# Kernel tuning notes

Measured on AMD Instinct MI355X. Metric: run time of the kernel, lower is better.

Reference implementation:

```python
import jax, jax.numpy as jnp
import numpy as np

WS = 7          # window_size
HEADS = 6
HEAD_DIM = 32
DISP = WS // 2  # displacement = 3
NEG = -1e9      # stands in for -inf in shift masks (safe for grads/low precision)


def _rel_indices():
    # get_relative_distances(window_size) + window_size - 1
    pos = np.array([[i, j] for i in range(WS) for j in range(WS)])  # (49, 2)
    return pos[None, :, :] - pos[:, None, :] + WS - 1               # (49, 49, 2)


def _shift_mask(nw_h, nw_w):
    # per-window additive mask replicating upper_lower_mask / left_right_mask placement
    n = WS * WS
    ul = np.zeros((n, n), np.float32)
    ul[-DISP * WS:, :-DISP * WS] = NEG
    ul[:-DISP * WS, -DISP * WS:] = NEG
    m4 = np.zeros((WS, WS, WS, WS), np.float32)
    m4[:, -DISP:, :, :-DISP] = NEG
    m4[:, :-DISP, :, -DISP:] = NEG
    lr = m4.reshape(n, n)
    full = np.zeros((nw_h, nw_w, n, n), np.float32)
    full[-1, :] += ul              # dots[:, :, -nw_w:] += upper_lower_mask
    full[:, -1] += lr              # dots[:, :, nw_w-1::nw_w] += left_right_mask
    return full.reshape(nw_h * nw_w, n, n)


def setup_inputs() -> dict:
    key = jax.random.key(0)
    k1, k2, k3, k4 = jax.random.split(key, 4)
    dim, inner = 192, HEADS * HEAD_DIM
    return {
        "x": jax.random.normal(k1, (16, 56, 56, dim), jnp.float32),
        "w_qkv": jax.random.normal(k2, (dim, inner * 3), jnp.float32) * 0.02,
        "pos_embedding": jax.random.normal(k3, (2 * WS - 1, 2 * WS - 1), jnp.float32),
        "w_out": jax.random.normal(k4, (inner, dim), jnp.float32) * 0.02,
        "b_out": jnp.zeros((dim,), jnp.float32),
    }


def reference(x, w_qkv, pos_embedding, w_out, b_out):
    b, H, W, dim = x.shape
    nw_h, nw_w = H // WS, W // WS
    x = jnp.roll(x, (-DISP, -DISP), axis=(1, 2))          # shifted window
    qkv = x @ w_qkv                                       # [b,H,W,3*inner]
    q, k, v = jnp.split(qkv, 3, axis=-1)

    def to_windows(t):  # [b,H,W,inner] -> [b,h,nw,ws*ws,d]
        t = t.reshape(b, nw_h, WS, nw_w, WS, HEADS, HEAD_DIM)
        return t.transpose(0, 5, 1, 3, 2, 4, 6).reshape(b, HEADS, nw_h * nw_w, WS * WS, HEAD_DIM)

    q, k, v = to_windows(q), to_windows(k), to_windows(v)
    scale = HEAD_DIM ** -0.5
    dots = jnp.einsum('bhwid,bhwjd->bhwij', q, k) * scale  # [b,h,nw,49,49]

    rel = _rel_indices()
    bias = pos_embedding[rel[..., 0], rel[..., 1]]         # [49,49]
    dots = dots + bias
    dots = dots + jnp.asarray(_shift_mask(nw_h, nw_w))     # broadcast over b,h

    attn = jax.nn.softmax(dots, axis=-1)
    out = jnp.einsum('bhwij,bhwjd->bhwid', attn, v)        # [b,h,nw,49,d]
    out = out.reshape(b, HEADS, nw_h, nw_w, WS, WS, HEAD_DIM)
    out = out.transpose(0, 2, 4, 3, 5, 1, 6).reshape(b, H, W, HEADS * HEAD_DIM)
    out = out @ w_out + b_out
    return jnp.roll(out, (DISP, DISP), axis=(1, 2))
```

## Files before the change

kernel.cpp:

```cpp
#include <hip/hip_runtime.h>
#include <hip/hip_bf16.h>

typedef __bf16 bf16_t;
typedef __bf16 bf16x8 __attribute__((ext_vector_type(8)));
typedef float f32x4 __attribute__((ext_vector_type(4)));
typedef unsigned int u32;

#define NB 16
#define HW 56
#define DIM 192
#define N3 576
#define WS7 7
#define HEADS 6
#define HD 32
#define NTOK 49
#define MFMA(a, b, c) __builtin_amdgcn_mfma_f32_16x16x32_bf16(a, b, c, 0, 0, 0)

__device__ __forceinline__ void gld_lds16(const bf16_t* g, bf16_t* l) {
    __builtin_amdgcn_global_load_lds((const __attribute__((address_space(1))) u32*)g,
                                     (__attribute__((address_space(3))) u32*)l, 16, 0, 0);
}

__global__ __launch_bounds__(256) void prep_x_kernel(const float* __restrict__ x,
                                                     bf16_t* __restrict__ xb) {
    int idx = blockIdx.x * 256 + threadIdx.x;
    const int total = NB * HW * HW * (DIM / 8);
    if (idx >= total) return;
    int c8 = idx % (DIM / 8);
    int p  = idx / (DIM / 8);
    int xx = p % HW;
    int yy = (p / HW) % HW;
    int bb = p / (HW * HW);
    int ys = yy + 3; if (ys >= HW) ys -= HW;
    int xs = xx + 3; if (xs >= HW) xs -= HW;
    const float* src = x + ((size_t)(bb * HW + ys) * HW + xs) * DIM + c8 * 8;
    float4 a0 = *reinterpret_cast<const float4*>(src);
    float4 a1 = *reinterpret_cast<const float4*>(src + 4);
    bf16x8 o;
    o[0] = (bf16_t)a0.x; o[1] = (bf16_t)a0.y; o[2] = (bf16_t)a0.z; o[3] = (bf16_t)a0.w;
    o[4] = (bf16_t)a1.x; o[5] = (bf16_t)a1.y; o[6] = (bf16_t)a1.z; o[7] = (bf16_t)a1.w;
    *reinterpret_cast<bf16x8*>(xb + (size_t)idx * 8) = o;
}

__global__ __launch_bounds__(256) void prep_w_kernel(const float* __restrict__ wqkv,
                                                     const float* __restrict__ wout,
                                                     bf16_t* __restrict__ wqkvt,
                                                     bf16_t* __restrict__ woutt) {
    int idx = blockIdx.x * 256 + threadIdx.x;
    if (idx < N3 * DIM) {
        int k = idx % DIM, n = idx / DIM;
        wqkvt[idx] = (bf16_t)wqkv[(size_t)k * N3 + n];
    } else {
        int j = idx - N3 * DIM;
        if (j < DIM * DIM) {
            int k = j % DIM, n = j / DIM;
            woutt[j] = (bf16_t)wout[(size_t)k * DIM + n];
        }
    }
}

__global__ __launch_bounds__(256) void prep_tbl_kernel(const float* __restrict__ pe,
                                                       float* __restrict__ tbl) {
    int idx = blockIdx.x * 256 + threadIdx.x;
    if (idx >= 4 * 64 * 64) return;
    int v = idx >> 12, rem = idx & 4095, ti = rem >> 6, tj = rem & 63;
    float val = -1e9f;
    if (ti < NTOK && tj < NTOK) {
        int yi = ti / 7, xi = ti % 7, yj = tj / 7, xj = tj % 7;
        val = pe[(yj - yi + 6) * 13 + (xj - xi + 6)];
        bool mr = (v & 2) && ((yi >= 4) != (yj >= 4));
        bool mc = (v & 1) && ((xi >= 4) != (xj >= 4));
        if (mr || mc) val = -1e9f;
    }
    tbl[idx] = val;
}

__global__ __launch_bounds__(256) void fused_attn_kernel2(const bf16_t* __restrict__ xb,
                                                          const bf16_t* __restrict__ wt,
                                                          const float* __restrict__ tbl,
                                                          bf16_t* __restrict__ att) {
    const int h = blockIdx.x, win = blockIdx.y, bb = blockIdx.z;
    const int wh = win >> 3, ww = win & 7;
    const int mt = threadIdx.x >> 6;
    const int lane = threadIdx.x & 63;
    const int lo = lane & 15, hi = lane >> 4;

    __shared__ alignas(16) bf16_t WL[96 * DIM];
    __shared__ alignas(16) bf16_t Qs[64 * 40];
    __shared__ alignas(16) bf16_t Ks[64 * 40];
    bf16_t* VTs = WL;
    bf16_t* P   = WL + 32 * 72;

#pragma unroll
    for (int i = 0; i < 9; i++) {
        int cbase = i * 256 + mt * 64;
        int cid = cbase + lane;
        int seg = cid / 768;
        int c0 = cid - seg * 768;
        int g0 = c0 ^ ((c0 / 24) & 7);
        gld_lds16(wt + (size_t)(seg * DIM + h * HD) * DIM + g0 * 8,
                  WL + (size_t)cbase * 8);
    }

    bf16x8 a[6];
    {
        int t = mt * 16 + lo;
        if (t >= NTOK) t = 0;
        int y = wh * WS7 + t / 7, xcol = ww * WS7 + t % 7;
        const bf16_t* ar = xb + ((size_t)(bb * HW + y) * HW + xcol) * DIM + hi * 8;
#pragma unroll
        for (int ks = 0; ks < 6; ks++)
            a[ks] = *reinterpret_cast<const bf16x8*>(ar + ks * 32);
    }

    __syncthreads();

    f32x4 acc6[3][2];
#pragma unroll
    for (int s = 0; s < 3; s++)
#pragma unroll
        for (int nt = 0; nt < 2; nt++) acc6[s][nt] = (f32x4){0.f, 0.f, 0.f, 0.f};

#pragma unroll
    for (int s = 0; s < 3; s++)
#pragma unroll
        for (int nt = 0; nt < 2; nt++) {
            int lr = s * 32 + nt * 16 + lo;
            const char* rowp = (const char*)WL + lr * 384;
            int rx = (lr & 7) << 4;
#pragma unroll
            for (int ks = 0; ks < 6; ks++) {
                bf16x8 bf = *reinterpret_cast<const bf16x8*>(rowp + ((ks * 64 + hi * 16) ^ rx));
                acc6[s][nt] = MFMA(a[ks], bf, acc6[s][nt]);
            }
        }

    __syncthreads();

    const float qs = 0.17677669529663687f;
#pragma unroll
    for (int nt = 0; nt < 2; nt++)
#pragma unroll
        for (int r = 0; r < 4; r++) {
            int tok = mt * 16 + hi * 4 + r;
            Qs[tok * 40 + nt * 16 + lo] = (bf16_t)(acc6[0][nt][r] * qs);
            Ks[tok * 40 + nt * 16 + lo] = (bf16_t)acc6[1][nt][r];
            VTs[(nt * 16 + lo) * 72 + tok] = (bf16_t)acc6[2][nt][r];
        }
    __syncthreads();

    const f32x4 zero4 = {0.f, 0.f, 0.f, 0.f};
    bf16x8 qa = *reinterpret_cast<const bf16x8*>(&Qs[(mt * 16 + lo) * 40 + hi * 8]);
    f32x4 s4[4];
#pragma unroll
    for (int ct = 0; ct < 4; ct++) {
        bf16x8 kb = *reinterpret_cast<const bf16x8*>(&Ks[(ct * 16 + lo) * 40 + hi * 8]);
        s4[ct] = MFMA(qa, kb, zero4);
    }

    const int variant = ((wh == 7) ? 2 : 0) | ((ww == 7) ? 1 : 0);
    const float* tbase = tbl + ((size_t)variant << 12);
    float rinv[4];
#pragma unroll
    for (int r = 0; r < 4; r++) {
        int ti = mt * 16 + hi * 4 + r;
        const float* trow = tbase + ti * 64 + lo;
        float vals[4];
        float mx = -3e38f;
#pragma unroll
        for (int ct = 0; ct < 4; ct++) {
            float v = s4[ct][r] + trow[ct * 16];
            vals[ct] = v;
            mx = fmaxf(mx, v);
        }
#pragma unroll
        for (int off = 1; off < 16; off <<= 1) mx = fmaxf(mx, __shfl_xor(mx, off));
        float sum = 0.f;
#pragma unroll
        for (int ct = 0; ct < 4; ct++) {
            float p = __expf(vals[ct] - mx);
            sum += p;
            P[ti * 72 + ct * 16 + lo] = (bf16_t)p;
        }
#pragma unroll
        for (int off = 1; off < 16; off <<= 1) sum += __shfl_xor(sum, off);
        rinv[r] = 1.f / sum;
    }

    f32x4 o[2] = {zero4, zero4};
#pragma unroll
    for (int ks = 0; ks < 2; ks++) {
        bf16x8 pa = *reinterpret_cast<const bf16x8*>(&P[(mt * 16 + lo) * 72 + ks * 32 + hi * 8]);
#pragma unroll
        for (int c2 = 0; c2 < 2; c2++) {
            bf16x8 vb = *reinterpret_cast<const bf16x8*>(&VTs[(c2 * 16 + lo) * 72 + ks * 32 + hi * 8]);
            o[c2] = MFMA(pa, vb, o[c2]);
        }
    }

#pragma unroll
    for (int r = 0; r < 4; r++) {
        int ti = mt * 16 + hi * 4 + r;
        if (ti < NTOK) {
            int y = wh * WS7 + ti / 7, xcol = ww * WS7 + ti % 7;
            size_t aoff = ((size_t)(bb * HW + y) * HW + xcol) * DIM + h * HD;
#pragma unroll
            for (int c2 = 0; c2 < 2; c2++)
                att[aoff + c2 * 16 + lo] = (bf16_t)(o[c2][r] * rinv[r]);
        }
    }
}

__global__ __launch_bounds__(256) void out_gemm2(const bf16_t* __restrict__ att,
                                                 const bf16_t* __restrict__ wt,
                                                 const float* __restrict__ bias,
                                                 float* __restrict__ out) {
    __shared__ alignas(16) bf16_t bsh[64 * DIM];
    const int mblk = blockIdx.x, nblk = blockIdx.y;
    const int wave = threadIdx.x >> 6, lane = threadIdx.x & 63;
    const int lo = lane & 15, hi = lane >> 4;

    const bf16_t* bt = wt + (size_t)nblk * 64 * DIM;
#pragma unroll
    for (int i = 0; i < 6; i++) {
        int s = wave * 384 + i * 64 + lane;
        int g = s ^ ((s / 24) & 7);
        gld_lds16(bt + g * 8, bsh + (wave * 384 + i * 64) * 8);
    }

    bf16x8 a[2][6];
    const bf16_t* ab = att + ((size_t)mblk * 128 + wave * 32 + lo) * DIM + hi * 8;
#pragma unroll
    for (int mt = 0; mt < 2; mt++)
#pragma unroll
        for (int ks = 0; ks < 6; ks++)
            a[mt][ks] = *reinterpret_cast<const bf16x8*>(ab + mt * 16 * DIM + ks * 32);

    f32x4 acc[2][4];
#pragma unroll
    for (int mt = 0; mt < 2; mt++)
#pragma unroll
        for (int ct = 0; ct < 4; ct++) acc[mt][ct] = (f32x4){0.f, 0.f, 0.f, 0.f};

    __syncthreads();

#pragma unroll
    for (int ks = 0; ks < 6; ks++)
#pragma unroll
        for (int ct = 0; ct < 4; ct++) {
            int r = ct * 16 + lo;
            int off = (ks * 64 + hi * 16) ^ ((r & 7) << 4);
            bf16x8 b = *reinterpret_cast<const bf16x8*>((const char*)bsh + r * 384 + off);
            acc[0][ct] = MFMA(a[0][ks], b, acc[0][ct]);
            acc[1][ct] = MFMA(a[1][ks], b, acc[1][ct]);
        }

    const int rb = mblk * 128 + wave * 32;
#pragma unroll
    for (int mt = 0; mt < 2; mt++)
#pragma unroll
        for (int r = 0; r < 4; r++) {
            int m = rb + mt * 16 + hi * 4 + r;
            int bb = m / (HW * HW);
            int rem = m - bb * HW * HW;
            int ya = rem / HW, xa = rem - ya * HW;
            int yo = ya + 3; if (yo >= HW) yo -= HW;
            int xo = xa + 3; if (xo >= HW) xo -= HW;
            size_t ob = ((size_t)(bb * HW + yo) * HW + xo) * DIM + nblk * 64;
#pragma unroll
            for (int ct = 0; ct < 4; ct++)
                out[ob + ct * 16 + lo] = acc[mt][ct][r] + bias[nblk * 64 + ct * 16 + lo];
        }
}

extern "C" void kernel_launch(void* const* d_in, const int* in_sizes, int n_in,
                              void* d_out, int out_size, void* d_ws, size_t ws_size,
                              hipStream_t stream) {
    const float* x    = (const float*)d_in[0];
    const float* wqkv = (const float*)d_in[1];
    const float* pe   = (const float*)d_in[2];
    const float* wout = (const float*)d_in[3];
    const float* bout = (const float*)d_in[4];
    float* out = (float*)d_out;

    char* ws = (char*)d_ws;
    const size_t XB_BYTES  = (size_t)NB * HW * HW * DIM * 2;
    const size_t ATT_BYTES = XB_BYTES;
    const size_t WQ_BYTES  = (size_t)N3 * DIM * 2;
    const size_t WO_BYTES  = (size_t)DIM * DIM * 2;
    bf16_t* xb    = (bf16_t*)ws;
    bf16_t* att   = (bf16_t*)(ws + XB_BYTES);
    bf16_t* wqkvt = (bf16_t*)(ws + XB_BYTES + ATT_BYTES);
    bf16_t* woutt = (bf16_t*)(ws + XB_BYTES + ATT_BYTES + WQ_BYTES);
    float*  tbl   = (float*)(ws + XB_BYTES + ATT_BYTES + WQ_BYTES + WO_BYTES);

    prep_x_kernel<<<(NB * HW * HW * (DIM / 8) + 255) / 256, 256, 0, stream>>>(x, xb);
    prep_w_kernel<<<(N3 * DIM + DIM * DIM + 255) / 256, 256, 0, stream>>>(wqkv, wout, wqkvt, woutt);
    prep_tbl_kernel<<<64, 256, 0, stream>>>(pe, tbl);
    fused_attn_kernel2<<<dim3(HEADS, 64, NB), 256, 0, stream>>>(xb, wqkvt, tbl, att);
    out_gemm2<<<dim3(392, 3), 256, 0, stream>>>(att, woutt, bout, out);
}
```

Baseline: 154.4 us.

## Process four windows per attention block and double output GEMM row tile

The fused attention kernel now loops over four windows per block. It loads the per-head K/V weights into LDS once and keeps the Q weights in registers, so weight staging is amortized across windows, and it prefetches the bias/mask table into registers. VTs and P get dedicated LDS buffers instead of aliasing the weight buffer. The output GEMM doubles its M tile to 256 rows per block, reusing each LDS B-fragment across four MFMA tiles. Grids shrink four-fold and two-fold, which reduces parallelism and raises register pressure.

```diff
diff --git a/kernel.cpp b/kernel.cpp
--- a/kernel.cpp
+++ b/kernel.cpp
@@ -75,143 +75,169 @@
     tbl[idx] = val;
 }
 
-__global__ __launch_bounds__(256) void fused_attn_kernel2(const bf16_t* __restrict__ xb,
+__global__ __launch_bounds__(256) void fused_attn_kernel3(const bf16_t* __restrict__ xb,
                                                           const bf16_t* __restrict__ wt,
                                                           const float* __restrict__ tbl,
                                                           bf16_t* __restrict__ att) {
-    const int h = blockIdx.x, win = blockIdx.y, bb = blockIdx.z;
-    const int wh = win >> 3, ww = win & 7;
+    const int h = blockIdx.x, wq = blockIdx.y, bb = blockIdx.z;
     const int mt = threadIdx.x >> 6;
     const int lane = threadIdx.x & 63;
     const int lo = lane & 15, hi = lane >> 4;
 
-    __shared__ alignas(16) bf16_t WL[96 * DIM];
+    __shared__ alignas(16) bf16_t WL[64 * DIM];
     __shared__ alignas(16) bf16_t Qs[64 * 40];
     __shared__ alignas(16) bf16_t Ks[64 * 40];
-    bf16_t* VTs = WL;
-    bf16_t* P   = WL + 32 * 72;
-
-#pragma unroll
-    for (int i = 0; i < 9; i++) {
+    __shared__ alignas(16) bf16_t VTs[32 * 72];
+    __shared__ alignas(16) bf16_t P[64 * 72];
+
+#pragma unroll
+    for (int i = 0; i < 6; i++) {
         int cbase = i * 256 + mt * 64;
         int cid = cbase + lane;
         int seg = cid / 768;
         int c0 = cid - seg * 768;
         int g0 = c0 ^ ((c0 / 24) & 7);
-        gld_lds16(wt + (size_t)(seg * DIM + h * HD) * DIM + g0 * 8,
+        gld_lds16(wt + (size_t)((seg + 1) * DIM + h * HD) * DIM + g0 * 8,
                   WL + (size_t)cbase * 8);
     }
 
-    bf16x8 a[6];
-    {
-        int t = mt * 16 + lo;
-        if (t >= NTOK) t = 0;
-        int y = wh * WS7 + t / 7, xcol = ww * WS7 + t % 7;
-        const bf16_t* ar = xb + ((size_t)(bb * HW + y) * HW + xcol) * DIM + hi * 8;
+    bf16x8 qw[2][6];
+#pragma unroll
+    for (int nt = 0; nt < 2; nt++) {
+        const bf16_t* bp = wt + (size_t)(h * HD + nt * 16 + lo) * DIM + hi * 8;
 #pragma unroll
         for (int ks = 0; ks < 6; ks++)
-            a[ks] = *reinterpret_cast<const bf16x8*>(ar + ks * 32);
+            qw[nt][ks] = *reinterpret_cast<const bf16x8*>(bp + ks * 32);
     }
 
     __syncthreads();
 
-    f32x4 acc6[3][2];
-#pragma unroll
-    for (int s = 0; s < 3; s++)
-#pragma unroll
-        for (int nt = 0; nt < 2; nt++) acc6[s][nt] = (f32x4){0.f, 0.f, 0.f, 0.f};
-
-#pragma unroll
-    for (int s = 0; s < 3; s++)
-#pragma unroll
-        for (int nt = 0; nt < 2; nt++) {
-            int lr = s * 32 + nt * 16 + lo;
-            const char* rowp = (const char*)WL + lr * 384;
-            int rx = (lr & 7) << 4;
-#pragma unroll
-            for (int ks = 0; ks < 6; ks++) {
-                bf16x8 bf = *reinterpret_cast<const bf16x8*>(rowp + ((ks * 64 + hi * 16) ^ rx));
-                acc6[s][nt] = MFMA(a[ks], bf, acc6[s][nt]);
-            }
-        }
-
-    __syncthreads();
-
     const float qs = 0.17677669529663687f;
-#pragma unroll
-    for (int nt = 0; nt < 2; nt++)
+    const f32x4 zero4 = {0.f, 0.f, 0.f, 0.f};
+
+    for (int w = 0; w < 4; w++) {
+        const int win = wq * 4 + w;
+        const int wh = win >> 3, ww = win & 7;
+
+        bf16x8 a[6];
+        {
+            int t = mt * 16 + lo;
+            if (t >= NTOK) t = 0;
+            int y = wh * WS7 + t / 7, xcol = ww * WS7 + t % 7;
+            const bf16_t* ar = xb + ((size_t)(bb * HW + y) * HW + xcol) * DIM + hi * 8;
+#pragma unroll
+            for (int ks = 0; ks < 6; ks++)
+                a[ks] = *reinterpret_cast<const bf16x8*>(ar + ks * 32);
+        }
+
+        const int variant = ((wh == 7) ? 2 : 0) | ((ww == 7) ? 1 : 0);
+        const float* tbase = tbl + ((size_t)variant << 12);
+        float tv[4][4];
+#pragma unroll
+        for (int r = 0; r < 4; r++)
+#pragma unroll
+            for (int ct = 0; ct < 4; ct++)
+                tv[r][ct] = tbase[(mt * 16 + hi * 4 + r) * 64 + ct * 16 + lo];
+
+        f32x4 acc6[3][2];
+#pragma unroll
+        for (int s = 0; s < 3; s++)
+#pragma unroll
+            for (int nt = 0; nt < 2; nt++) acc6[s][nt] = zero4;
+
+#pragma unroll
+        for (int nt = 0; nt < 2; nt++)
+#pragma unroll
+            for (int ks = 0; ks < 6; ks++)
+                acc6[0][nt] = MFMA(a[ks], qw[nt][ks], acc6[0][nt]);
+
+#pragma unroll
+        for (int s = 1; s < 3; s++)
+#pragma unroll
+            for (int nt = 0; nt < 2; nt++) {
+                int lr = (s - 1) * 32 + nt * 16 + lo;
+                const char* rowp = (const char*)WL + lr * 384;
+                int rx = (lr & 7) << 4;
+#pragma unroll
+                for (int ks = 0; ks < 6; ks++) {
+                    bf16x8 bf = *reinterpret_cast<const bf16x8*>(rowp + ((ks * 64 + hi * 16) ^ rx));
+                    acc6[s][nt] = MFMA(a[ks], bf, acc6[s][nt]);
+                }
+            }
+
+        __syncthreads();
+
+#pragma unroll
+        for (int nt = 0; nt < 2; nt++)
+#pragma unroll
+            for (int r = 0; r < 4; r++) {
+                int tok = mt * 16 + hi * 4 + r;
+                Qs[tok * 40 + nt * 16 + lo] = (bf16_t)(acc6[0][nt][r] * qs);
+                Ks[tok * 40 + nt * 16 + lo] = (bf16_t)acc6[1][nt][r];
+                VTs[(nt * 16 + lo) * 72 + tok] = (bf16_t)acc6[2][nt][r];
+            }
+        __syncthreads();
+
+        bf16x8 qa = *reinterpret_cast<const bf16x8*>(&Qs[(mt * 16 + lo) * 40 + hi * 8]);
+        f32x4 s4[4];
+#pragma unroll
+        for (int ct = 0; ct < 4; ct++) {
+            bf16x8 kb = *reinterpret_cast<const bf16x8*>(&Ks[(ct * 16 + lo) * 40 + hi * 8]);
+            s4[ct] = MFMA(qa, kb, zero4);
+        }
+
+        float rinv[4];
 #pragma unroll
         for (int r = 0; r < 4; r++) {
-            int tok = mt * 16 + hi * 4 + r;
-            Qs[tok * 40 + nt * 16 + lo] = (bf16_t)(acc6[0][nt][r] * qs);
-            Ks[tok * 40 + nt * 16 + lo] = (bf16_t)acc6[1][nt][r];
-            VTs[(nt * 16 + lo) * 72 + tok] = (bf16_t)acc6[2][nt][r];
-        }
-    __syncthreads();
-
-    const f32x4 zero4 = {0.f, 0.f, 0.f, 0.f};
-    bf16x8 qa = *reinterpret_cast<const bf16x8*>(&Qs[(mt * 16 + lo) * 40 + hi * 8]);
-    f32x4 s4[4];
-#pragma unroll
-    for (int ct = 0; ct < 4; ct++) {
-        bf16x8 kb = *reinterpret_cast<const bf16x8*>(&Ks[(ct * 16 + lo) * 40 + hi * 8]);
-        s4[ct] = MFMA(qa, kb, zero4);
-    }
-
-    const int variant = ((wh == 7) ? 2 : 0) | ((ww == 7) ? 1 : 0);
-    const float* tbase = tbl + ((size_t)variant << 12);
-    float rinv[4];
-#pragma unroll
-    for (int r = 0; r < 4; r++) {
-        int ti = mt * 16 + hi * 4 + r;
-        const float* trow = tbase + ti * 64 + lo;
-        float vals[4];
-        float mx = -3e38f;
-#pragma unroll
-        for (int ct = 0; ct < 4; ct++) {
-            float v = s4[ct][r] + trow[ct * 16];
-            vals[ct] = v;
-            mx = fmaxf(mx, v);
-        }
-#pragma unroll
-        for (int off = 1; off < 16; off <<= 1) mx = fmaxf(mx, __shfl_xor(mx, off));
-        float sum = 0.f;
-#pragma unroll
-        for (int ct = 0; ct < 4; ct++) {
-            float p = __expf(vals[ct] - mx);
-            sum += p;
-            P[ti * 72 + ct * 16 + lo] = (bf16_t)p;
-        }
-#pragma unroll
-        for (int off = 1; off < 16; off <<= 1) sum += __shfl_xor(sum, off);
-        rinv[r] = 1.f / sum;
-    }
-
-    f32x4 o[2] = {zero4, zero4};
-#pragma unroll
-    for (int ks = 0; ks < 2; ks++) {
-        bf16x8 pa = *reinterpret_cast<const bf16x8*>(&P[(mt * 16 + lo) * 72 + ks * 32 + hi * 8]);
-#pragma unroll
-        for (int c2 = 0; c2 < 2; c2++) {
-            bf16x8 vb = *reinterpret_cast<const bf16x8*>(&VTs[(c2 * 16 + lo) * 72 + ks * 32 + hi * 8]);
-            o[c2] = MFMA(pa, vb, o[c2]);
-        }
-    }
-
-#pragma unroll
-    for (int r = 0; r < 4; r++) {
-        int ti = mt * 16 + hi * 4 + r;
-        if (ti < NTOK) {
-            int y = wh * WS7 + ti / 7, xcol = ww * WS7 + ti % 7;
-            size_t aoff = ((size_t)(bb * HW + y) * HW + xcol) * DIM + h * HD;
-#pragma unroll
-            for (int c2 = 0; c2 < 2; c2++)
-                att[aoff + c2 * 16 + lo] = (bf16_t)(o[c2][r] * rinv[r]);
-        }
-    }
-}
-
-__global__ __launch_bounds__(256) void out_gemm2(const bf16_t* __restrict__ att,
+            int ti = mt * 16 + hi * 4 + r;
+            float vals[4];
+            float mx = -3e38f;
+#pragma unroll
+            for (int ct = 0; ct < 4; ct++) {
+                float v = s4[ct][r] + tv[r][ct];
+                vals[ct] = v;
+                mx = fmaxf(mx, v);
+            }
+#pragma unroll
+            for (int off = 1; off < 16; off <<= 1) mx = fmaxf(mx, __shfl_xor(mx, off));
+            float sum = 0.f;
+#pragma unroll
+            for (int ct = 0; ct < 4; ct++) {
+                float p = __expf(vals[ct] - mx);
+                sum += p;
+                P[ti * 72 + ct * 16 + lo] = (bf16_t)p;
+            }
+#pragma unroll
+            for (int off = 1; off < 16; off <<= 1) sum += __shfl_xor(sum, off);
+            rinv[r] = 1.f / sum;
+        }
+
+        f32x4 o[2] = {zero4, zero4};
+#pragma unroll
+        for (int ks = 0; ks < 2; ks++) {
+            bf16x8 pa = *reinterpret_cast<const bf16x8*>(&P[(mt * 16 + lo) * 72 + ks * 32 + hi * 8]);
+#pragma unroll
+            for (int c2 = 0; c2 < 2; c2++) {
+                bf16x8 vb = *reinterpret_cast<const bf16x8*>(&VTs[(c2 * 16 + lo) * 72 + ks * 32 + hi * 8]);
+                o[c2] = MFMA(pa, vb, o[c2]);
+            }
+        }
+
+#pragma unroll
+        for (int r = 0; r < 4; r++) {
+            int ti = mt * 16 + hi * 4 + r;
+            if (ti < NTOK) {
+                int y = wh * WS7 + ti / 7, xcol = ww * WS7 + ti % 7;
+                size_t aoff = ((size_t)(bb * HW + y) * HW + xcol) * DIM + h * HD;
+#pragma unroll
+                for (int c2 = 0; c2 < 2; c2++)
+                    att[aoff + c2 * 16 + lo] = (bf16_t)(o[c2][r] * rinv[r]);
+            }
+        }
+    }
+}
+
+__global__ __launch_bounds__(256) void out_gemm3(const bf16_t* __restrict__ att,
                                                  const bf16_t* __restrict__ wt,
                                                  const float* __restrict__ bias,
                                                  float* __restrict__ out) {
@@ -228,17 +254,17 @@
         gld_lds16(bt + g * 8, bsh + (wave * 384 + i * 64) * 8);
     }
 
-    bf16x8 a[2][6];
-    const bf16_t* ab = att + ((size_t)mblk * 128 + wave * 32 + lo) * DIM + hi * 8;
-#pragma unroll
-    for (int mt = 0; mt < 2; mt++)
+    bf16x8 a[4][6];
+    const bf16_t* ab = att + ((size_t)mblk * 256 + wave * 64 + lo) * DIM + hi * 8;
+#pragma unroll
+    for (int mt = 0; mt < 4; mt++)
 #pragma unroll
         for (int ks = 0; ks < 6; ks++)
             a[mt][ks] = *reinterpret_cast<const bf16x8*>(ab + mt * 16 * DIM + ks * 32);
 
-    f32x4 acc[2][4];
-#pragma unroll
-    for (int mt = 0; mt < 2; mt++)
+    f32x4 acc[4][4];
+#pragma unroll
+    for (int mt = 0; mt < 4; mt++)
 #pragma unroll
         for (int ct = 0; ct < 4; ct++) acc[mt][ct] = (f32x4){0.f, 0.f, 0.f, 0.f};
 
@@ -251,13 +277,14 @@
             int r = ct * 16 + lo;
             int off = (ks * 64 + hi * 16) ^ ((r & 7) << 4);
             bf16x8 b = *reinterpret_cast<const bf16x8*>((const char*)bsh + r * 384 + off);
-            acc[0][ct] = MFMA(a[0][ks], b, acc[0][ct]);
-            acc[1][ct] = MFMA(a[1][ks], b, acc[1][ct]);
-        }
-
-    const int rb = mblk * 128 + wave * 32;
-#pragma unroll
-    for (int mt = 0; mt < 2; mt++)
+#pragma unroll
+            for (int mt = 0; mt < 4; mt++)
+                acc[mt][ct] = MFMA(a[mt][ks], b, acc[mt][ct]);
+        }
+
+    const int rb = mblk * 256 + wave * 64;
+#pragma unroll
+    for (int mt = 0; mt < 4; mt++)
 #pragma unroll
         for (int r = 0; r < 4; r++) {
             int m = rb + mt * 16 + hi * 4 + r;
@@ -297,6 +324,6 @@
     prep_x_kernel<<<(NB * HW * HW * (DIM / 8) + 255) / 256, 256, 0, stream>>>(x, xb);
     prep_w_kernel<<<(N3 * DIM + DIM * DIM + 255) / 256, 256, 0, stream>>>(wqkv, wout, wqkvt, woutt);
     prep_tbl_kernel<<<64, 256, 0, stream>>>(pe, tbl);
-    fused_attn_kernel2<<<dim3(HEADS, 64, NB), 256, 0, stream>>>(xb, wqkvt, tbl, att);
-    out_gemm2<<<dim3(392, 3), 256, 0, stream>>>(att, woutt, bout, out);
-}
+    fused_attn_kernel3<<<dim3(HEADS, 16, NB), 256, 0, stream>>>(xb, wqkvt, tbl, att);
+    out_gemm3<<<dim3(196, 3), 256, 0, stream>>>(att, woutt, bout, out);
+}
```

Result: slower. 163.8 us (+6.1%).
